# Performance work log

Measured on AMD Instinct MI355X. Metric: run time of the kernel, lower is better.

The kernel has to match this reference:

```python
import jax, jax.numpy as jnp
import numpy as np
from jax import lax

TAU = 20.0
DT = 1.0
THRESH = 1.0

# Hard-threshold spike with surrogate gradient (triangular window around thresh),
# matching torch SpikeFunction.
@jax.custom_vjp
def spike(v):
    return (v >= THRESH).astype(v.dtype)

def _spike_fwd(v):
    return spike(v), v

def _spike_bwd(v, g):
    return (g * jnp.clip(1.0 - jnp.abs(v - THRESH), 0.0, 1.0),)

spike.defvjp(_spike_fwd, _spike_bwd)


def setup_inputs() -> dict:
    key = jax.random.key(0)
    B, F, T = 64, 2048, 512
    x = jax.random.normal(key, (B, F, T), dtype=jnp.float32)
    return {"x": x}


def reference(x) -> jnp.ndarray:
    # x: [B, F, T]; sequential LIF membrane scan over T with spike + hard reset.
    B, F, T = x.shape

    def step(v, x_t):
        v = v + (x_t - v) * (DT / TAU)
        s = spike(v)
        v = v * (1.0 - s)  # reset-to-zero on spike
        return v, s

    x_tmajor = jnp.moveaxis(x, 2, 0)  # [T, B, F]
    v0 = jnp.zeros((B, F), dtype=x.dtype)
    _, spikes = lax.scan(step, v0, x_tmajor)  # spikes: [T, B, F]
    return jnp.moveaxis(spikes, 0, 2)  # [B, F, T]
```

## Files before the change

### kernel.cpp

```cpp
#include <hip/hip_runtime.h>


#define T_LEN 512
#define CHUNK 64
#define NCHUNK (T_LEN / CHUNK)

__global__ __launch_bounds__(64, 2)
void lif_kernel(const float* __restrict__ x, float* __restrict__ out) {
    __shared__ float tile[CHUNK][64];
    const int lane = threadIdx.x;
    const size_t row0 = (size_t)blockIdx.x * 64;
    const float kk = 1.0f / 20.0f;
    float v = 0.0f;

    const float* xb = x + row0 * T_LEN;
    float* ob = out + row0 * T_LEN;

    const int rL = lane >> 4;
    const int cL = (lane & 15) * 4;

    float4 buf[16];

    #pragma unroll
    for (int p = 0; p < 16; ++p) {
        const int r = p * 4 + rL;
        buf[p] = *reinterpret_cast<const float4*>(xb + (size_t)r * T_LEN + cL);
    }

    for (int ch = 0; ch < NCHUNK; ++ch) {
        #pragma unroll
        for (int p = 0; p < 16; ++p) {
            const int r = p * 4 + rL;
            tile[cL + 0][r ^ (cL + 0)] = buf[p].x;
            tile[cL + 1][r ^ (cL + 1)] = buf[p].y;
            tile[cL + 2][r ^ (cL + 2)] = buf[p].z;
            tile[cL + 3][r ^ (cL + 3)] = buf[p].w;
        }

        if (ch + 1 < NCHUNK) {
            const float* xc = xb + (size_t)(ch + 1) * CHUNK;
            #pragma unroll
            for (int p = 0; p < 16; ++p) {
                const int r = p * 4 + rL;
                buf[p] = *reinterpret_cast<const float4*>(xc + (size_t)r * T_LEN + cL);
            }
        }

        asm volatile("s_waitcnt lgkmcnt(0)" ::: "memory");

        #pragma unroll
        for (int t = 0; t < CHUNK; ++t) {
            const float xv = tile[t][lane ^ t];
            v = v + (xv - v) * kk;
            const bool fire = (v >= 1.0f);
            tile[t][lane ^ t] = fire ? 1.0f : 0.0f;
            v = fire ? 0.0f : v;
        }

        asm volatile("s_waitcnt lgkmcnt(0)" ::: "memory");

        float* oc = ob + (size_t)ch * CHUNK;
        #pragma unroll
        for (int p = 0; p < 16; ++p) {
            const int r = p * 4 + rL;
            float4 s;
            s.x = tile[cL + 0][r ^ (cL + 0)];
            s.y = tile[cL + 1][r ^ (cL + 1)];
            s.z = tile[cL + 2][r ^ (cL + 2)];
            s.w = tile[cL + 3][r ^ (cL + 3)];
            *reinterpret_cast<float4*>(oc + (size_t)r * T_LEN + cL) = s;
        }

        asm volatile("s_waitcnt lgkmcnt(0)" ::: "memory");
    }
}

extern "C" void kernel_launch(void* const* d_in, const int* in_sizes, int n_in,
                              void* d_out, int out_size, void* d_ws, size_t ws_size,
                              hipStream_t stream) {
    const float* x = (const float*)d_in[0];
    float* out = (float*)d_out;
    const int rows = in_sizes[0] / T_LEN;
    const int grid = rows / 64;
    lif_kernel<<<dim3(grid), dim3(64), 0, stream>>>(x, out);
}
```

Measured before the change: 441.9 us.

## Double-buffer input prefetch, write zeros nontemporally and scatter sparse spike ones

After: 451.8 us. +2.2%, slower.

```diff
diff --git a/kernel.cpp b/kernel.cpp
--- a/kernel.cpp
+++ b/kernel.cpp
@@ -1,5 +1,7 @@
 #include <hip/hip_runtime.h>
 
+
+typedef float f4 __attribute__((ext_vector_type(4)));
 
 #define T_LEN 512
 #define CHUNK 64
@@ -19,60 +21,82 @@
     const int rL = lane >> 4;
     const int cL = (lane & 15) * 4;
 
-    float4 buf[16];
+    f4 bufA[16], bufB[16];
+    const f4 zero4 = {0.f, 0.f, 0.f, 0.f};
 
     #pragma unroll
     for (int p = 0; p < 16; ++p) {
         const int r = p * 4 + rL;
-        buf[p] = *reinterpret_cast<const float4*>(xb + (size_t)r * T_LEN + cL);
+        bufA[p] = __builtin_nontemporal_load(
+            (const f4*)(xb + (size_t)r * T_LEN + cL));
+    }
+    #pragma unroll
+    for (int p = 0; p < 16; ++p) {
+        const int r = p * 4 + rL;
+        bufB[p] = __builtin_nontemporal_load(
+            (const f4*)(xb + (size_t)r * T_LEN + CHUNK + cL));
     }
 
-    for (int ch = 0; ch < NCHUNK; ++ch) {
-        #pragma unroll
-        for (int p = 0; p < 16; ++p) {
-            const int r = p * 4 + rL;
-            tile[cL + 0][r ^ (cL + 0)] = buf[p].x;
-            tile[cL + 1][r ^ (cL + 1)] = buf[p].y;
-            tile[cL + 2][r ^ (cL + 2)] = buf[p].z;
-            tile[cL + 3][r ^ (cL + 3)] = buf[p].w;
-        }
+#define STEP(CH, BUF)                                                         \
+    {                                                                         \
+                          \
+        asm volatile("s_waitcnt lgkmcnt(0)" ::: "memory");                    \
+        _Pragma("unroll")                                                     \
+        for (int p = 0; p < 16; ++p) {            \
+            const int r = p * 4 + rL;                                         \
+            tile[cL + 0][r ^ (cL + 0)] = BUF[p][0];                           \
+            tile[cL + 1][r ^ (cL + 1)] = BUF[p][1];                           \
+            tile[cL + 2][r ^ (cL + 2)] = BUF[p][2];                           \
+            tile[cL + 3][r ^ (cL + 3)] = BUF[p][3];                           \
+        }                                                                     \
+        if ((CH) + 2 < NCHUNK) {                     \
+            const float* xc = xb + (size_t)((CH) + 2) * CHUNK;                \
+            _Pragma("unroll")                                                 \
+            for (int p = 0; p < 16; ++p) {                                    \
+                const int r = p * 4 + rL;                                     \
+                BUF[p] = __builtin_nontemporal_load(                          \
+                    (const f4*)(xc + (size_t)r * T_LEN + cL));                \
+            }                                                                 \
+        }                                                                     \
+        {                                    \
+            float* oc = ob + (size_t)(CH) * CHUNK;                            \
+            _Pragma("unroll")                                                 \
+            for (int p = 0; p < 16; ++p) {                                    \
+                const int r = p * 4 + rL;                                     \
+                __builtin_nontemporal_store(                                  \
+                    zero4, (f4*)(oc + (size_t)r * T_LEN + cL));               \
+            }                                                                 \
+        }                                                                     \
+        asm volatile("s_waitcnt lgkmcnt(0)" ::: "memory");                    \
+        unsigned long long spk = 0ull;                                        \
+        _Pragma("unroll")                                                     \
+        for (int t = 0; t < CHUNK; ++t) {        \
+            const float xv = tile[t][lane ^ t];                               \
+            v = v + (xv - v) * kk;                                            \
+            const bool fire = (v >= 1.0f);                                    \
+            spk |= ((unsigned long long)fire) << t;                           \
+            v = fire ? 0.0f : v;                                              \
+        }                                                                     \
+        if (spk) {                        \
+            asm volatile("s_waitcnt vmcnt(0)" ::: "memory");                  \
+            float* orow = out + (row0 + lane) * T_LEN + (size_t)(CH) * CHUNK; \
+            while (spk) {                                                     \
+                const int t = __builtin_ctzll(spk);                           \
+                spk &= spk - 1;                                               \
+                orow[t] = 1.0f;                                               \
+            }                                                                 \
+        }                                                                     \
+    }
 
-        if (ch + 1 < NCHUNK) {
-            const float* xc = xb + (size_t)(ch + 1) * CHUNK;
-            #pragma unroll
-            for (int p = 0; p < 16; ++p) {
-                const int r = p * 4 + rL;
-                buf[p] = *reinterpret_cast<const float4*>(xc + (size_t)r * T_LEN + cL);
-            }
-        }
-
-        asm volatile("s_waitcnt lgkmcnt(0)" ::: "memory");
-
-        #pragma unroll
-        for (int t = 0; t < CHUNK; ++t) {
-            const float xv = tile[t][lane ^ t];
-            v = v + (xv - v) * kk;
-            const bool fire = (v >= 1.0f);
-            tile[t][lane ^ t] = fire ? 1.0f : 0.0f;
-            v = fire ? 0.0f : v;
-        }
-
-        asm volatile("s_waitcnt lgkmcnt(0)" ::: "memory");
-
-        float* oc = ob + (size_t)ch * CHUNK;
-        #pragma unroll
-        for (int p = 0; p < 16; ++p) {
-            const int r = p * 4 + rL;
-            float4 s;
-            s.x = tile[cL + 0][r ^ (cL + 0)];
-            s.y = tile[cL + 1][r ^ (cL + 1)];
-            s.z = tile[cL + 2][r ^ (cL + 2)];
-            s.w = tile[cL + 3][r ^ (cL + 3)];
-            *reinterpret_cast<float4*>(oc + (size_t)r * T_LEN + cL) = s;
-        }
-
-        asm volatile("s_waitcnt lgkmcnt(0)" ::: "memory");
-    }
+    STEP(0, bufA)
+    STEP(1, bufB)
+    STEP(2, bufA)
+    STEP(3, bufB)
+    STEP(4, bufA)
+    STEP(5, bufB)
+    STEP(6, bufA)
+    STEP(7, bufB)
+#undef STEP
 }
 
 extern "C" void kernel_launch(void* const* d_in, const int* in_sizes, int n_in,
```
